# Kernel tuning notes

Measured on AMD Instinct MI355X. Metric: run time of the kernel, lower is better.

## Reference

```python
import jax, jax.numpy as jnp
import numpy as np

BN_EPS = 1e-5


def _bn_train(x, gamma, beta):
    # torch BatchNorm1d in training mode: normalize with batch mean and
    # biased batch variance.
    mu = jnp.mean(x, axis=0)
    var = jnp.var(x, axis=0)
    return (x - mu) * jax.lax.rsqrt(var + BN_EPS) * gamma + beta


def setup_inputs() -> dict:
    key = jax.random.key(0)
    ks = jax.random.split(key, 12)
    N, F_D, F_C, E, VOCAB, H = 16384, 26, 10, 16, 200000, 400
    D_IN = (F_D + F_C) * E  # 576
    return {
        "Xi_dense": jax.random.normal(ks[0], (N, F_D, 1), jnp.float32),
        "Xv": jax.random.uniform(ks[1], (N, F_D + F_C), jnp.float32),
        "Wd": jax.random.normal(ks[2], (F_D, E), jnp.float32) * 0.1,
        "bd": jax.random.normal(ks[3], (F_D, E), jnp.float32) * 0.1,
        "tables": jax.random.normal(ks[4], (F_C, VOCAB, E), jnp.float32) * 0.1,
        "W1": jax.random.normal(ks[5], (H, D_IN), jnp.float32) * 0.05,
        "b1": jax.random.normal(ks[6], (H,), jnp.float32) * 0.05,
        "g1": jnp.ones((H,), jnp.float32),
        "be1": jnp.zeros((H,), jnp.float32),
        "W2": jax.random.normal(ks[7], (H, H), jnp.float32) * 0.05,
        "b2": jax.random.normal(ks[8], (H,), jnp.float32) * 0.05,
        "g2": jnp.ones((H,), jnp.float32),
        "be2": jnp.zeros((H,), jnp.float32),
        "bias_vec": jax.random.normal(ks[9], (N,), jnp.float32),
        "Xi_cat": jax.random.randint(ks[10], (N, F_C, 1), 0, VOCAB, jnp.int32),
    }


def reference(Xi_dense, Xv, Wd, bd, tables, W1, b1, g1, be1,
              W2, b2, g2, be2, bias_vec, Xi_cat):
    N = Xi_dense.shape[0]
    # dense fields: per-field Linear(1, E) -> x * W + b, shape (N, 26, E)
    dense_emb = Xi_dense * Wd[None] + bd[None]  # (N,26,1)*(1,26,E) broadcast
    # categorical fields: per-field embedding lookup, shape (N, 10, E)
    cat_emb = jax.vmap(lambda tbl, idx: tbl[idx], in_axes=(0, 1), out_axes=1)(
        tables, Xi_cat[:, :, 0])
    # scale each field embedding by its Xv value
    all_emb = jnp.concatenate([dense_emb, cat_emb], axis=1) * Xv[:, :, None]  # (N,36,E)

    # fm first order: concat of all scaled field embeddings
    fm_first = all_emb.reshape(N, -1)  # (N, 576)
    # fm second order: 0.5 * ((sum)^2 - sum of squares)
    s = jnp.sum(all_emb, axis=1)                       # (N, E)
    fm_second = 0.5 * (s * s - jnp.sum(all_emb * all_emb, axis=1))  # (N, E)

    # deep part: Linear -> BatchNorm (train-mode stats) per hidden layer;
    # dropout p=0 -> identity.
    deep = fm_first
    deep = _bn_train(deep @ W1.T + b1, g1, be1)
    deep = _bn_train(deep @ W2.T + b2, g2, be2)

    total = (jnp.sum(fm_first, axis=1) + jnp.sum(fm_second, axis=1)
             + jnp.sum(deep, axis=1) + bias_vec)
    return total
```

## Files before the change

### kernel.cpp

```cpp
#include <hip/hip_runtime.h>

#define BN_EPS 1e-5f

typedef unsigned short u16;
typedef __attribute__((ext_vector_type(8))) short bf16x8;
typedef __attribute__((ext_vector_type(4))) float f32x4;

__device__ __forceinline__ u16 f2bf(float x) {
  union { float f; unsigned int u; } v; v.f = x;
  unsigned int r = v.u + 0x7fffu + ((v.u >> 16) & 1u);
  return (u16)(r >> 16);
}
__device__ __forceinline__ float bf2f(u16 h) {
  union { unsigned int u; float f; } v; v.u = ((unsigned int)h) << 16;
  return v.f;
}

__device__ __forceinline__ float wave_reduce_sum(float v) {
#pragma unroll
  for (int off = 1; off < 64; off <<= 1) v += __shfl_xor(v, off, 64);
  return v;
}

__device__ __forceinline__ void gload_lds16(const void* g, void* l) {
  __builtin_amdgcn_global_load_lds(
      (const __attribute__((address_space(1))) void*)g,
      (__attribute__((address_space(3))) void*)l, 16, 0, 0);
}

__global__ __launch_bounds__(256) void embed_prep(
    const float* __restrict__ Xi_dense, const float* __restrict__ Xv,
    const float* __restrict__ Wd, const float* __restrict__ bd,
    const float* __restrict__ tables, const int* __restrict__ Xi_cat,
    const float* __restrict__ bias_vec, const float* __restrict__ W1,
    u16* __restrict__ fm_first, float* __restrict__ partial,
    u16* __restrict__ W1h, float* __restrict__ statz) {
  const int t = threadIdx.x;
  if (blockIdx.x >= 512) {
    const int bb = blockIdx.x - 512;
    if (bb == 0) {
#pragma unroll
      for (int i = 0; i < 8; ++i) statz[i * 256 + t] = 0.f;
    }
    const int base = bb * 4096;
#pragma unroll
    for (int e = 0; e < 16; ++e) {
      const int idx = base + e * 256 + t;
      const int r = idx / 576;
      const int j = idx - r * 576;
      W1h[idx] = (r < 400) ? f2bf(W1[r * 576 + j]) : (u16)0;
    }
    return;
  }

  __shared__ float Xvs[32 * 37];
  __shared__ float Xds[32 * 27];
  __shared__ int Cis[32 * 11];
  __shared__ float Wds[416], Bds[416];
  const int n0 = blockIdx.x * 32;

  for (int i = t; i < 1152; i += 256) {
    const int r = i / 36;
    Xvs[r * 37 + (i - r * 36)] = Xv[n0 * 36 + i];
  }
  for (int i = t; i < 832; i += 256) {
    const int r = i / 26;
    Xds[r * 27 + (i - r * 26)] = Xi_dense[n0 * 26 + i];
  }
  for (int i = t; i < 320; i += 256) {
    const int r = i / 10;
    Cis[r * 11 + (i - r * 10)] = Xi_cat[n0 * 10 + i];
  }
  for (int i = t; i < 416; i += 256) {
    Wds[i] = Wd[i];
    Bds[i] = bd[i];
  }
  __syncthreads();

  const int r = t >> 3, q = t & 7;
  const int n = n0 + r;
  const int fbase = q >> 1, eh = (q & 1) * 8;
  float s8[8] = {}, q8[8] = {};
  float sum_all = 0.f;
  u16* frow = fm_first + (size_t)n * 576;

#pragma unroll
  for (int j = 0; j < 9; ++j) {
    const int f = fbase + 4 * j;
    const float xvv = Xvs[r * 37 + f];
    float val[8];
    if (f < 26) {
      const float xd = Xds[r * 27 + f];
      const float4 w0 = *(const float4*)&Wds[f * 16 + eh];
      const float4 w1 = *(const float4*)&Wds[f * 16 + eh + 4];
      const float4 b0 = *(const float4*)&Bds[f * 16 + eh];
      const float4 b1v = *(const float4*)&Bds[f * 16 + eh + 4];
      val[0] = fmaf(xd, w0.x, b0.x) * xvv;
      val[1] = fmaf(xd, w0.y, b0.y) * xvv;
      val[2] = fmaf(xd, w0.z, b0.z) * xvv;
      val[3] = fmaf(xd, w0.w, b0.w) * xvv;
      val[4] = fmaf(xd, w1.x, b1v.x) * xvv;
      val[5] = fmaf(xd, w1.y, b1v.y) * xvv;
      val[6] = fmaf(xd, w1.z, b1v.z) * xvv;
      val[7] = fmaf(xd, w1.w, b1v.w) * xvv;
    } else {
      const int fc = f - 26;
      const int row = Cis[r * 11 + fc];
      const float* tp =
          tables + ((size_t)fc * 200000 + (size_t)row) * 16 + eh;
      const float4 v0 = *(const float4*)tp;
      const float4 v1 = *(const float4*)(tp + 4);
      val[0] = v0.x * xvv;
      val[1] = v0.y * xvv;
      val[2] = v0.z * xvv;
      val[3] = v0.w * xvv;
      val[4] = v1.x * xvv;
      val[5] = v1.y * xvv;
      val[6] = v1.z * xvv;
      val[7] = v1.w * xvv;
    }
    bf16x8 o;
#pragma unroll
    for (int jj = 0; jj < 8; ++jj) {
      s8[jj] += val[jj];
      q8[jj] += val[jj] * val[jj];
      sum_all += val[jj];
      o[jj] = (short)f2bf(val[jj]);
    }
    *(bf16x8*)&frow[f * 16 + eh] = o;
  }

  float fm2h = 0.f;
#pragma unroll
  for (int jj = 0; jj < 8; ++jj) {
    float se = s8[jj] + __shfl_xor(s8[jj], 2, 64);
    se += __shfl_xor(se, 4, 64);
    float qe = q8[jj] + __shfl_xor(q8[jj], 2, 64);
    qe += __shfl_xor(qe, 4, 64);
    fm2h += se * se - qe;
  }
  const float fm2 = 0.5f * (fm2h + __shfl_xor(fm2h, 1, 64));
  float srow = sum_all + __shfl_xor(sum_all, 1, 64);
  srow += __shfl_xor(srow, 2, 64);
  srow += __shfl_xor(srow, 4, 64);
  if (q == 0) partial[n] = srow + fm2 + bias_vec[n];
}

template <int NFR>
__device__ __forceinline__ void gemm_body(
    const u16* __restrict__ A, int lda, const u16* __restrict__ W, int ldw,
    u16* __restrict__ Y, int ldc, int Ncap, float* __restrict__ aS,
    float* __restrict__ aQ, int K, int bx, int by, u16 (*As)[64 * 32],
    u16 (*Bs)[128 * 32], float (&rS)[2][4][2][16],
    float (&rQ)[2][4][2][16]) {
  const int t = threadIdx.x;
  const int bm = bx * 64;
  const int bn = by * 128;
  const int wid = t >> 6, lane = t & 63;
  const int wr = wid >> 1, wc = wid & 1;
  const int lr = lane & 15;
  const int sr = lane >> 2;
  const int ssw = (((lane & 3) ^ ((sr >> 1) & 3))) * 8;
  const int lkS = (((lane >> 4) ^ ((lr >> 1) & 3))) * 8;
  const bool active = (NFR == 4) || (wc == 0);

  f32x4 acc[2][NFR] = {};

  auto STAGE = [&](int buf, int kt) {
    gload_lds16(&A[(size_t)(bm + wid * 16 + sr) * lda + kt + ssw],
                &As[buf][wid * 512]);
#pragma unroll
    for (int i = 0; i < 2; ++i) {
      const int c = (NFR == 4) ? (wid * 2 + i) : i;
      gload_lds16(&W[(size_t)(bn + c * 16 + sr) * ldw + kt + ssw],
                  &Bs[buf][c * 512]);
    }
  };

  auto COMPUTE = [&](int buf) {
    if (active) {
      bf16x8 af[2], bfv[NFR];
#pragma unroll
      for (int mf = 0; mf < 2; ++mf)
        af[mf] = *(const bf16x8*)&As[buf][(wr * 32 + mf * 16 + lr) * 32 + lkS];
#pragma unroll
      for (int nf = 0; nf < NFR; ++nf)
        bfv[nf] =
            *(const bf16x8*)&Bs[buf][(wc * 64 + nf * 16 + lr) * 32 + lkS];
      __builtin_amdgcn_s_setprio(1);
#pragma unroll
      for (int mf = 0; mf < 2; ++mf)
#pragma unroll
        for (int nf = 0; nf < NFR; ++nf)
          acc[mf][nf] = __builtin_amdgcn_mfma_f32_16x16x32_bf16(
              af[mf], bfv[nf], acc[mf][nf], 0, 0, 0);
      __builtin_amdgcn_s_setprio(0);
    }
  };

  STAGE(0, 0);
  int cur = 0;
  for (int kt = 32; kt < K; kt += 32) {
    STAGE(cur ^ 1, kt);
    asm volatile("s_waitcnt vmcnt(3)" ::: "memory");
    __builtin_amdgcn_s_barrier();
    COMPUTE(cur);
    __builtin_amdgcn_s_barrier();
    cur ^= 1;
  }
  asm volatile("s_waitcnt vmcnt(0)" ::: "memory");
  __builtin_amdgcn_s_barrier();
  COMPUTE(cur);

  const int l4 = (lane >> 4) * 4;
  __syncthreads();
  if (active) {
#pragma unroll
    for (int nf = 0; nf < NFR; ++nf) {
      const int col = bn + wc * 64 + nf * 16 + lr;
      float s = 0.f, q = 0.f;
#pragma unroll
      for (int mf = 0; mf < 2; ++mf) {
#pragma unroll
        for (int r = 0; r < 4; ++r) {
          const int row = bm + wr * 32 + mf * 16 + l4 + r;
          const float v = acc[mf][nf][r];
          s += v;
          q += v * v;
          if (col < Ncap) Y[(size_t)row * ldc + col] = f2bf(v);
        }
      }
      s += __shfl_xor(s, 16, 64);
      s += __shfl_xor(s, 32, 64);
      q += __shfl_xor(q, 16, 64);
      q += __shfl_xor(q, 32, 64);
      if (lane < 16) {
        rS[wc][nf][wr][lr] = s;
        rQ[wc][nf][wr][lr] = q;
      }
    }
  }
  __syncthreads();
  if (t < (NFR == 4 ? 128 : 32)) {
    const int wcc = t >> 6, nff = (t >> 4) & 3, c = t & 15;
    atomicAdd(&aS[bn + t], rS[wcc][nff][0][c] + rS[wcc][nff][1][c]);
    atomicAdd(&aQ[bn + t], rQ[wcc][nff][0][c] + rQ[wcc][nff][1][c]);
  }
}

__global__ __launch_bounds__(256) void gemm_bf16(
    const u16* __restrict__ A, int lda,
    const u16* __restrict__ W, int ldw,
    u16* __restrict__ Y, int ldc, int Ncap,
    float* __restrict__ aS, float* __restrict__ aQ, int K) {
  __shared__ u16 As[2][64 * 32];
  __shared__ u16 Bs[2][128 * 32];
  __shared__ float rS[2][4][2][16];
  __shared__ float rQ[2][4][2][16];
  const int bid = blockIdx.x;
  const int l = (bid & 7) * (gridDim.x >> 3) + (bid >> 3);
  const int bx = l >> 2, by = l & 3;
  if (by < 3)
    gemm_body<4>(A, lda, W, ldw, Y, ldc, Ncap, aS, aQ, K, bx, by, As, Bs,
                 rS, rQ);
  else
    gemm_body<2>(A, lda, W, ldw, Y, ldc, Ncap, aS, aQ, K, bx, by, As, Bs,
                 rS, rQ);
}

__global__ __launch_bounds__(256) void prep2(
    const float* __restrict__ aS1, const float* __restrict__ aQ1,
    const float* __restrict__ g1, const float* __restrict__ W2,
    u16* __restrict__ W2p) {
  const int c = blockIdx.x * 256 + threadIdx.x;
  const int row = c / 104;
  const int jc = (c - row * 104) * 4;
  ushort4 o = {0, 0, 0, 0};
  if (row < 400 && jc < 400) {
    const float4 S = *(const float4*)&aS1[jc];
    const float4 Q = *(const float4*)&aQ1[jc];
    const float4 G = *(const float4*)&g1[jc];
    const float4 w = *(const float4*)&W2[(size_t)row * 400 + jc];
    const float inv = 1.f / 16384.f;
    float mu, var, a;
    mu = S.x * inv; var = Q.x * inv - mu * mu;
    a = G.x * rsqrtf(var + BN_EPS); o.x = f2bf(w.x * a);
    mu = S.y * inv; var = Q.y * inv - mu * mu;
    a = G.y * rsqrtf(var + BN_EPS); o.y = f2bf(w.y * a);
    mu = S.z * inv; var = Q.z * inv - mu * mu;
    a = G.z * rsqrtf(var + BN_EPS); o.z = f2bf(w.z * a);
    mu = S.w * inv; var = Q.w * inv - mu * mu;
    a = G.w * rsqrtf(var + BN_EPS); o.w = f2bf(w.w * a);
  }
  *(ushort4*)&W2p[(size_t)row * 416 + jc] = o;
}

__device__ __forceinline__ void bn_affine4(const float* aS, const float* aQ,
                                           const float* g, const float* be,
                                           int j, float4& aa, float4& cc) {
  const float4 S = *(const float4*)&aS[j];
  const float4 Q = *(const float4*)&aQ[j];
  const float4 G = *(const float4*)&g[j];
  const float4 E = *(const float4*)&be[j];
  const float inv = 1.f / 16384.f;
  float mu, var;
  mu = S.x * inv; var = Q.x * inv - mu * mu;
  aa.x = G.x * rsqrtf(var + BN_EPS); cc.x = E.x - mu * aa.x;
  mu = S.y * inv; var = Q.y * inv - mu * mu;
  aa.y = G.y * rsqrtf(var + BN_EPS); cc.y = E.y - mu * aa.y;
  mu = S.z * inv; var = Q.z * inv - mu * mu;
  aa.z = G.z * rsqrtf(var + BN_EPS); cc.z = E.z - mu * aa.z;
  mu = S.w * inv; var = Q.w * inv - mu * mu;
  aa.w = G.w * rsqrtf(var + BN_EPS); cc.w = E.w - mu * aa.w;
}

__global__ __launch_bounds__(256) void final_kernel(
    const u16* __restrict__ Y2, const float* __restrict__ aS2,
    const float* __restrict__ aQ2, const float* __restrict__ g2,
    const float* __restrict__ be2, const float* __restrict__ partial,
    float* __restrict__ out) {
  const int t = threadIdx.x;
  const int lane = t & 63;
  const int wid = t >> 6;
  const int j0 = lane * 8;
  float ar[8], cr[8];
  if (j0 < 400) {
    float4 aa0, cc0, aa1, cc1;
    bn_affine4(aS2, aQ2, g2, be2, j0, aa0, cc0);
    bn_affine4(aS2, aQ2, g2, be2, j0 + 4, aa1, cc1);
    ar[0] = aa0.x; ar[1] = aa0.y; ar[2] = aa0.z; ar[3] = aa0.w;
    ar[4] = aa1.x; ar[5] = aa1.y; ar[6] = aa1.z; ar[7] = aa1.w;
    cr[0] = cc0.x; cr[1] = cc0.y; cr[2] = cc0.z; cr[3] = cc0.w;
    cr[4] = cc1.x; cr[5] = cc1.y; cr[6] = cc1.z; cr[7] = cc1.w;
  } else {
#pragma unroll
    for (int k = 0; k < 8; ++k) { ar[k] = 0.f; cr[k] = 0.f; }
  }
#pragma unroll
  for (int r = 0; r < 4; ++r) {
    const int n = blockIdx.x * 16 + wid * 4 + r;
    float acc = 0.f;
    if (j0 < 400) {
      const bf16x8 y = *(const bf16x8*)&Y2[(size_t)n * 400 + j0];
#pragma unroll
      for (int k = 0; k < 8; ++k)
        acc += fmaf(ar[k], bf2f((u16)y[k]), cr[k]);
    }
    acc = wave_reduce_sum(acc);
    if (lane == 0) out[n] = partial[n] + acc;
  }
}

extern "C" void kernel_launch(void* const* d_in, const int* in_sizes, int n_in,
                              void* d_out, int out_size, void* d_ws,
                              size_t ws_size, hipStream_t stream) {
  const float* Xi_dense = (const float*)d_in[0];
  const float* Xv = (const float*)d_in[1];
  const float* Wd = (const float*)d_in[2];
  const float* bd = (const float*)d_in[3];
  const float* tables = (const float*)d_in[4];
  const float* W1 = (const float*)d_in[5];
  const float* g1 = (const float*)d_in[7];
  const float* W2 = (const float*)d_in[9];
  const float* g2 = (const float*)d_in[11];
  const float* be2 = (const float*)d_in[12];
  const float* bias_vec = (const float*)d_in[13];
  const int* Xi_cat = (const int*)d_in[14];

  constexpr int N = 16384;
  constexpr int DIN = 576;
  constexpr int H = 400;
  constexpr int KP = 416;
  constexpr int WPAD = 512;
  constexpr int NXB = 256;

  u16* fm_first = (u16*)d_ws;
  u16* Y1h = fm_first + (size_t)N * DIN;
  u16* Y2h = Y1h + (size_t)N * KP;
  u16* W1h = Y2h + (size_t)N * H;
  u16* W2p = W1h + (size_t)WPAD * DIN;
  float* fptr = (float*)(W2p + (size_t)WPAD * KP);
  float* partial = fptr;
  float* aS1 = partial + N;
  float* aQ1 = aS1 + WPAD;
  float* aS2 = aQ1 + WPAD;
  float* aQ2 = aS2 + WPAD;

  embed_prep<<<512 + 72, 256, 0, stream>>>(Xi_dense, Xv, Wd, bd, tables,
                                           Xi_cat, bias_vec, W1, fm_first,
                                           partial, W1h, aS1);

  gemm_bf16<<<NXB * 4, 256, 0, stream>>>(fm_first, DIN, W1h, DIN,
                                         Y1h, KP, KP, aS1, aQ1, DIN);

  prep2<<<208, 256, 0, stream>>>(aS1, aQ1, g1, W2, W2p);

  gemm_bf16<<<NXB * 4, 256, 0, stream>>>(Y1h, KP, W2p, KP,
                                         Y2h, H, H, aS2, aQ2, KP);

  final_kernel<<<N / 16, 256, 0, stream>>>(Y2h, aS2, aQ2, g2, be2, partial,
                                           (float*)d_out);
}
```

Baseline: 66.61 us.

## Enlarge GEMM block tile to 128x128 with K-step 64 and pad K to 448

The bf16 MFMA GEMM moves from a 64x128 block tile with a K-step of 32 to a 128x128 tile with a K-step of 64. Each wave now computes a 64x64 sub-tile, and the global-to-LDS staging and XOR swizzle are redone to match. The special narrow path for the last column tile is removed, and the hidden padding KP grows to 448 so K divides evenly by 64. The aim is more reuse of A and B per LDS load and fewer loop iterations and barriers. The cost is twice the LDS use, more accumulator registers, and wasted MFMA work on padded columns 400–511.

Result: faster. 57.88 us, median of 2 (-13.1%).

```diff
diff --git a/kernel.cpp b/kernel.cpp
--- a/kernel.cpp
+++ b/kernel.cpp
@@ -146,126 +146,111 @@
   if (q == 0) partial[n] = srow + fm2 + bias_vec[n];
 }
 
-template <int NFR>
-__device__ __forceinline__ void gemm_body(
-    const u16* __restrict__ A, int lda, const u16* __restrict__ W, int ldw,
-    u16* __restrict__ Y, int ldc, int Ncap, float* __restrict__ aS,
-    float* __restrict__ aQ, int K, int bx, int by, u16 (*As)[64 * 32],
-    u16 (*Bs)[128 * 32], float (&rS)[2][4][2][16],
-    float (&rQ)[2][4][2][16]) {
-  const int t = threadIdx.x;
-  const int bm = bx * 64;
-  const int bn = by * 128;
-  const int wid = t >> 6, lane = t & 63;
-  const int wr = wid >> 1, wc = wid & 1;
-  const int lr = lane & 15;
-  const int sr = lane >> 2;
-  const int ssw = (((lane & 3) ^ ((sr >> 1) & 3))) * 8;
-  const int lkS = (((lane >> 4) ^ ((lr >> 1) & 3))) * 8;
-  const bool active = (NFR == 4) || (wc == 0);
-
-  f32x4 acc[2][NFR] = {};
-
-  auto STAGE = [&](int buf, int kt) {
-    gload_lds16(&A[(size_t)(bm + wid * 16 + sr) * lda + kt + ssw],
-                &As[buf][wid * 512]);
-#pragma unroll
-    for (int i = 0; i < 2; ++i) {
-      const int c = (NFR == 4) ? (wid * 2 + i) : i;
-      gload_lds16(&W[(size_t)(bn + c * 16 + sr) * ldw + kt + ssw],
-                  &Bs[buf][c * 512]);
-    }
-  };
-
-  auto COMPUTE = [&](int buf) {
-    if (active) {
-      bf16x8 af[2], bfv[NFR];
-#pragma unroll
-      for (int mf = 0; mf < 2; ++mf)
-        af[mf] = *(const bf16x8*)&As[buf][(wr * 32 + mf * 16 + lr) * 32 + lkS];
-#pragma unroll
-      for (int nf = 0; nf < NFR; ++nf)
-        bfv[nf] =
-            *(const bf16x8*)&Bs[buf][(wc * 64 + nf * 16 + lr) * 32 + lkS];
-      __builtin_amdgcn_s_setprio(1);
-#pragma unroll
-      for (int mf = 0; mf < 2; ++mf)
-#pragma unroll
-        for (int nf = 0; nf < NFR; ++nf)
-          acc[mf][nf] = __builtin_amdgcn_mfma_f32_16x16x32_bf16(
-              af[mf], bfv[nf], acc[mf][nf], 0, 0, 0);
-      __builtin_amdgcn_s_setprio(0);
-    }
-  };
-
-  STAGE(0, 0);
-  int cur = 0;
-  for (int kt = 32; kt < K; kt += 32) {
-    STAGE(cur ^ 1, kt);
-    asm volatile("s_waitcnt vmcnt(3)" ::: "memory");
-    __builtin_amdgcn_s_barrier();
-    COMPUTE(cur);
-    __builtin_amdgcn_s_barrier();
-    cur ^= 1;
-  }
-  asm volatile("s_waitcnt vmcnt(0)" ::: "memory");
-  __builtin_amdgcn_s_barrier();
-  COMPUTE(cur);
-
-  const int l4 = (lane >> 4) * 4;
-  __syncthreads();
-  if (active) {
-#pragma unroll
-    for (int nf = 0; nf < NFR; ++nf) {
-      const int col = bn + wc * 64 + nf * 16 + lr;
-      float s = 0.f, q = 0.f;
-#pragma unroll
-      for (int mf = 0; mf < 2; ++mf) {
-#pragma unroll
-        for (int r = 0; r < 4; ++r) {
-          const int row = bm + wr * 32 + mf * 16 + l4 + r;
-          const float v = acc[mf][nf][r];
-          s += v;
-          q += v * v;
-          if (col < Ncap) Y[(size_t)row * ldc + col] = f2bf(v);
-        }
-      }
-      s += __shfl_xor(s, 16, 64);
-      s += __shfl_xor(s, 32, 64);
-      q += __shfl_xor(q, 16, 64);
-      q += __shfl_xor(q, 32, 64);
-      if (lane < 16) {
-        rS[wc][nf][wr][lr] = s;
-        rQ[wc][nf][wr][lr] = q;
-      }
-    }
-  }
-  __syncthreads();
-  if (t < (NFR == 4 ? 128 : 32)) {
-    const int wcc = t >> 6, nff = (t >> 4) & 3, c = t & 15;
-    atomicAdd(&aS[bn + t], rS[wcc][nff][0][c] + rS[wcc][nff][1][c]);
-    atomicAdd(&aQ[bn + t], rQ[wcc][nff][0][c] + rQ[wcc][nff][1][c]);
-  }
-}
-
 __global__ __launch_bounds__(256) void gemm_bf16(
     const u16* __restrict__ A, int lda,
     const u16* __restrict__ W, int ldw,
     u16* __restrict__ Y, int ldc, int Ncap,
     float* __restrict__ aS, float* __restrict__ aQ, int K) {
-  __shared__ u16 As[2][64 * 32];
-  __shared__ u16 Bs[2][128 * 32];
+  __shared__ u16 As[2][128 * 64];
+  __shared__ u16 Bs[2][128 * 64];
   __shared__ float rS[2][4][2][16];
   __shared__ float rQ[2][4][2][16];
+
+  const int t = threadIdx.x;
   const int bid = blockIdx.x;
   const int l = (bid & 7) * (gridDim.x >> 3) + (bid >> 3);
   const int bx = l >> 2, by = l & 3;
-  if (by < 3)
-    gemm_body<4>(A, lda, W, ldw, Y, ldc, Ncap, aS, aQ, K, bx, by, As, Bs,
-                 rS, rQ);
-  else
-    gemm_body<2>(A, lda, W, ldw, Y, ldc, Ncap, aS, aQ, K, bx, by, As, Bs,
-                 rS, rQ);
+  const int bm = bx * 128, bn = by * 128;
+  const int wid = t >> 6, lane = t & 63;
+  const int wr = wid >> 1, wc = wid & 1;
+  const int lr = lane & 15, hi = lane >> 4;
+  const int sr = lane >> 3;
+  const int sl = ((lane & 7) ^ sr) * 8;
+
+  f32x4 acc[4][4] = {};
+
+  auto STAGE = [&](int buf, int kt) {
+#pragma unroll
+    for (int i = 0; i < 8; ++i) {
+      const int c = (wid & 1) * 8 + i;
+      if (wid < 2)
+        gload_lds16(&A[(size_t)(bm + c * 8 + sr) * lda + kt + sl],
+                    &As[buf][c * 512]);
+      else
+        gload_lds16(&W[(size_t)(bn + c * 8 + sr) * ldw + kt + sl],
+                    &Bs[buf][c * 512]);
+    }
+  };
+
+  auto COMPUTE = [&](int buf) {
+#pragma unroll
+    for (int ks = 0; ks < 2; ++ks) {
+      const int ps = ((ks * 4 + hi) ^ (lr & 7)) * 8;
+      bf16x8 af[4], bfv[4];
+#pragma unroll
+      for (int mf = 0; mf < 4; ++mf)
+        af[mf] = *(const bf16x8*)&As[buf][(wr * 64 + mf * 16 + lr) * 64 + ps];
+#pragma unroll
+      for (int nf = 0; nf < 4; ++nf)
+        bfv[nf] =
+            *(const bf16x8*)&Bs[buf][(wc * 64 + nf * 16 + lr) * 64 + ps];
+      __builtin_amdgcn_s_setprio(1);
+#pragma unroll
+      for (int mf = 0; mf < 4; ++mf)
+#pragma unroll
+        for (int nf = 0; nf < 4; ++nf)
+          acc[mf][nf] = __builtin_amdgcn_mfma_f32_16x16x32_bf16(
+              af[mf], bfv[nf], acc[mf][nf], 0, 0, 0);
+      __builtin_amdgcn_s_setprio(0);
+    }
+  };
+
+  STAGE(0, 0);
+  int cur = 0;
+  for (int kt = 64; kt < K; kt += 64) {
+    STAGE(cur ^ 1, kt);
+    asm volatile("s_waitcnt vmcnt(8)" ::: "memory");
+    __builtin_amdgcn_s_barrier();
+    COMPUTE(cur);
+    __builtin_amdgcn_s_barrier();
+    cur ^= 1;
+  }
+  asm volatile("s_waitcnt vmcnt(0)" ::: "memory");
+  __builtin_amdgcn_s_barrier();
+  COMPUTE(cur);
+
+  const int l4 = hi * 4;
+  __syncthreads();
+#pragma unroll
+  for (int nf = 0; nf < 4; ++nf) {
+    const int col = bn + wc * 64 + nf * 16 + lr;
+    float s = 0.f, q = 0.f;
+#pragma unroll
+    for (int mf = 0; mf < 4; ++mf) {
+#pragma unroll
+      for (int r = 0; r < 4; ++r) {
+        const int row = bm + wr * 64 + mf * 16 + l4 + r;
+        const float v = acc[mf][nf][r];
+        s += v;
+        q += v * v;
+        if (col < Ncap) Y[(size_t)row * ldc + col] = f2bf(v);
+      }
+    }
+    s += __shfl_xor(s, 16, 64);
+    s += __shfl_xor(s, 32, 64);
+    q += __shfl_xor(q, 16, 64);
+    q += __shfl_xor(q, 32, 64);
+    if (lane < 16) {
+      rS[wc][nf][wr][lr] = s;
+      rQ[wc][nf][wr][lr] = q;
+    }
+  }
+  __syncthreads();
+  if (t < 128) {
+    const int wcc = t >> 6, nff = (t >> 4) & 3, c = t & 15;
+    atomicAdd(&aS[bn + t], rS[wcc][nff][0][c] + rS[wcc][nff][1][c]);
+    atomicAdd(&aQ[bn + t], rQ[wcc][nff][0][c] + rQ[wcc][nff][1][c]);
+  }
 }
 
 __global__ __launch_bounds__(256) void prep2(
@@ -273,8 +258,8 @@
     const float* __restrict__ g1, const float* __restrict__ W2,
     u16* __restrict__ W2p) {
   const int c = blockIdx.x * 256 + threadIdx.x;
-  const int row = c / 104;
-  const int jc = (c - row * 104) * 4;
+  const int row = c / 112;
+  const int jc = (c - row * 112) * 4;
   ushort4 o = {0, 0, 0, 0};
   if (row < 400 && jc < 400) {
     const float4 S = *(const float4*)&aS1[jc];
@@ -292,7 +277,7 @@
     mu = S.w * inv; var = Q.w * inv - mu * mu;
     a = G.w * rsqrtf(var + BN_EPS); o.w = f2bf(w.w * a);
   }
-  *(ushort4*)&W2p[(size_t)row * 416 + jc] = o;
+  *(ushort4*)&W2p[(size_t)row * 448 + jc] = o;
 }
 
 __device__ __forceinline__ void bn_affine4(const float* aS, const float* aQ,
@@ -370,9 +355,8 @@
   constexpr int N = 16384;
   constexpr int DIN = 576;
   constexpr int H = 400;
-  constexpr int KP = 416;
+  constexpr int KP = 448;
   constexpr int WPAD = 512;
-  constexpr int NXB = 256;
 
   u16* fm_first = (u16*)d_ws;
   u16* Y1h = fm_first + (size_t)N * DIN;
@@ -390,13 +374,13 @@
                                            Xi_cat, bias_vec, W1, fm_first,
                                            partial, W1h, aS1);
 
-  gemm_bf16<<<NXB * 4, 256, 0, stream>>>(fm_first, DIN, W1h, DIN,
-                                         Y1h, KP, KP, aS1, aQ1, DIN);
-
-  prep2<<<208, 256, 0, stream>>>(aS1, aQ1, g1, W2, W2p);
-
-  gemm_bf16<<<NXB * 4, 256, 0, stream>>>(Y1h, KP, W2p, KP,
-                                         Y2h, H, H, aS2, aQ2, KP);
+  gemm_bf16<<<512, 256, 0, stream>>>(fm_first, DIN, W1h, DIN,
+                                     Y1h, KP, KP, aS1, aQ1, DIN);
+
+  prep2<<<224, 256, 0, stream>>>(aS1, aQ1, g1, W2, W2p);
+
+  gemm_bf16<<<512, 256, 0, stream>>>(Y1h, KP, W2p, KP,
+                                     Y2h, H, H, aS2, aQ2, KP);
 
   final_kernel<<<N / 16, 256, 0, stream>>>(Y2h, aS2, aQ2, g2, be2, partial,
                                            (float*)d_out);
```
